# Kernel tuning notes

Measured on AMD Instinct MI355X. Metric: run time of the kernel, lower is better.

Reference implementation:

```python
import jax, jax.numpy as jnp
import numpy as np

HEAD = 3
EMB = 192
MAX_LAYER = 4
NEG_SLOPE_ATT = 0.2
NEG_SLOPE_ACT = 0.1
BN_EPS = 1e-5

def leaky_relu(x, slope):
    return jnp.where(x >= 0, x, slope * x)

def setup_inputs() -> dict:
    key = jax.random.key(0)
    ks = jax.random.split(key, 8)
    N, E, D_IN = 64000, 512000, 128
    k = EMB // HEAD
    subx = jax.random.normal(ks[0], (N, D_IN), dtype=jnp.float32)
    edge_index = jax.random.randint(ks[1], (2, E), 0, N, dtype=jnp.int32)
    mask = jax.random.randint(ks[2], (E, 1), 0, 2, dtype=jnp.int32)
    W = jax.random.normal(ks[3], (EMB, D_IN), dtype=jnp.float32) * (1.0 / np.sqrt(D_IN))
    att = jax.random.normal(ks[4], (1, HEAD, 2 * k), dtype=jnp.float32) * 0.1
    bias = jnp.zeros((EMB,), dtype=jnp.float32)
    gamma = jnp.ones((EMB,), dtype=jnp.float32)
    beta = jnp.zeros((EMB,), dtype=jnp.float32)
    return {"subx": subx, "edge_index": edge_index, "mask": mask, "W": W,
            "att": att, "bias": bias, "gamma": gamma, "beta": beta,
            "batch_size": 32, "subgraph_size": 500}

def reference(subx, edge_index, mask, W, att, bias, gamma, beta, batch_size, subgraph_size):
    N = subx.shape[0]
    k = EMB // HEAD
    # linear projection, split into heads: [N, H, k]
    x = (subx @ W.T).reshape(N, HEAD, k)
    src = edge_index[0]  # softmax grouping index (as in original code)
    dst = edge_index[1]  # aggregation target (PyG source_to_target flow)
    x_i = x[dst]  # [E, H, k]
    x_j = x[src]  # [E, H, k]
    # attention logits per edge per head
    alpha = (jnp.concatenate([x_i, x_j], axis=-1) * att).sum(-1)  # [E, H]
    alpha = leaky_relu(alpha, NEG_SLOPE_ATT)
    # segment softmax grouped by src (faithful to original)
    amax = jax.ops.segment_max(alpha, src, num_segments=N)
    ex = jnp.exp(alpha - amax[src])
    denom = jax.ops.segment_sum(ex, src, num_segments=N)
    alpha = ex / (denom[src] + 1e-16)
    # edge mask (tile over heads)
    m = (mask.reshape(-1, 1, 1) != 0)
    msg = jnp.where(m, x_j, 0.0) * alpha[..., None]  # [E, H, k]
    # scatter-add to target nodes
    aggr = jax.ops.segment_sum(msg, dst, num_segments=N).reshape(N, EMB) + bias
    # LeakyReLU(0.1) then BatchNorm1d (training-mode batch stats)
    h = leaky_relu(aggr, NEG_SLOPE_ACT)
    mean = h.mean(axis=0)
    var = h.var(axis=0)
    h = gamma * (h - mean) / jnp.sqrt(var + BN_EPS) + beta
    # mean over k-hop layers
    h = h.reshape(batch_size, MAX_LAYER, subgraph_size, EMB)
    return h.mean(axis=1)
```

## Files before the change

### kernel.cpp

```cpp
#include <hip/hip_runtime.h>

#define EMBD 192
#define DIN 128
#define SB 1024

__device__ __forceinline__ void f4add(float4& a, const float4& b){
  a.x += b.x; a.y += b.y; a.z += b.z; a.w += b.w;
}

__global__ __launch_bounds__(256) void k_gemm(const float* __restrict__ A,
      const float* __restrict__ W, const float* __restrict__ att,
      float* __restrict__ X, float* __restrict__ ai4, float* __restrict__ aj4,
      unsigned* __restrict__ zbuf, long zcount, int N){
  {
    long i = (long)(blockIdx.y*gridDim.x + blockIdx.x)*blockDim.x + threadIdx.x;
    long st = (long)gridDim.x*gridDim.y*blockDim.x;
    for (; i < zcount; i += st) zbuf[i] = 0u;
  }

  __shared__ float4 Ws[2048];
  int t  = threadIdx.x;
  int nb = blockIdx.y;
  const float4* Wg = (const float4*)W + (size_t)nb*2048;
  #pragma unroll
  for (int i = 0; i < 8; i++){
    int idx = i*256 + t;
    int wr = idx >> 5, wk = idx & 31;
    Ws[wr*32 + (wk ^ ((wr>>3)&7))] = Wg[idx];
  }

  int c = t & 7;
  int r = t >> 3;
  float atti[8], attj[8];
  #pragma unroll
  for (int j = 0; j < 8; j++){
    atti[j] = att[nb*128 + c*8 + j];
    attj[j] = att[nb*128 + 64 + c*8 + j];
  }
  __syncthreads();

  int m0 = blockIdx.x*128 + r*4;
  int mc0 = (m0 + 3 < N) ? m0 : (N > 4 ? N - 4 : 0);
  const float4* Ag = (const float4*)A;

  float acc[4][8];
  #pragma unroll
  for (int rr = 0; rr < 4; rr++)
    #pragma unroll
    for (int j = 0; j < 8; j++) acc[rr][j] = 0.f;

  float4 a_cur[4];
  #pragma unroll
  for (int rr = 0; rr < 4; rr++) a_cur[rr] = Ag[(size_t)(mc0+rr)*32];

  #pragma unroll 4
  for (int k4 = 0; k4 < 32; k4++){
    float4 a_nxt[4];
    if (k4 < 31){
      #pragma unroll
      for (int rr = 0; rr < 4; rr++) a_nxt[rr] = Ag[(size_t)(mc0+rr)*32 + k4 + 1];
    }
    #pragma unroll
    for (int j = 0; j < 8; j++){
      float4 w = Ws[(c*8 + j)*32 + (k4 ^ c)];
      #pragma unroll
      for (int rr = 0; rr < 4; rr++){
        acc[rr][j] += a_cur[rr].x*w.x + a_cur[rr].y*w.y + a_cur[rr].z*w.z + a_cur[rr].w*w.w;
      }
    }
    #pragma unroll
    for (int rr = 0; rr < 4; rr++) a_cur[rr] = a_nxt[rr];
  }

  #pragma unroll
  for (int rr = 0; rr < 4; rr++){
    int m = mc0 + rr;
    float pi = 0.f, pj = 0.f;
    #pragma unroll
    for (int j = 0; j < 8; j++){ pi += acc[rr][j]*atti[j]; pj += acc[rr][j]*attj[j]; }
    pi += __shfl_xor(pi, 1); pi += __shfl_xor(pi, 2); pi += __shfl_xor(pi, 4);
    pj += __shfl_xor(pj, 1); pj += __shfl_xor(pj, 2); pj += __shfl_xor(pj, 4);
    if (m0 + rr < N){
      float4* Xo = (float4*)(X + (size_t)m*EMBD + nb*64 + c*8);
      Xo[0] = make_float4(acc[rr][0], acc[rr][1], acc[rr][2], acc[rr][3]);
      Xo[1] = make_float4(acc[rr][4], acc[rr][5], acc[rr][6], acc[rr][7]);
      if (c == 0){ ai4[(size_t)m*4 + nb] = pi; aj4[(size_t)m*4 + nb] = pj; }
    }
  }
}

__global__ void k_count(const int* __restrict__ ei, const int* __restrict__ msk,
    int* __restrict__ count2, int* __restrict__ slot_src, int* __restrict__ slot_dst,
    int E, int N){
  int e = blockIdx.x*256 + threadIdx.x;
  if (e >= E) return;
  int s = ei[e], d = ei[E + e];
  slot_src[e] = atomicAdd(&count2[s], 1);
  slot_dst[e] = msk[e] ? atomicAdd(&count2[N + d], 1) : -1;
}

__global__ void k_scan1(const int* __restrict__ count, int* __restrict__ offs,
                        int* __restrict__ bsum, int M){
  __shared__ int sm[256];
  int t = threadIdx.x, i = blockIdx.x*256 + t;
  int v = (i < M) ? count[i] : 0;
  sm[t] = v; __syncthreads();
  for (int o = 1; o < 256; o <<= 1){
    int u = (t >= o) ? sm[t-o] : 0;
    __syncthreads();
    sm[t] += u;
    __syncthreads();
  }
  if (i < M) offs[i] = sm[t] - v;
  if (t == 255) bsum[blockIdx.x] = sm[255];
}

__global__ void k_scan2(int* __restrict__ bsum, int NB){
  __shared__ int sm[1024];
  int t = threadIdx.x;
  int v = (t < NB) ? bsum[t] : 0;
  sm[t] = v; __syncthreads();
  for (int o = 1; o < 1024; o <<= 1){
    int u = (t >= o) ? sm[t-o] : 0;
    __syncthreads();
    sm[t] += u;
    __syncthreads();
  }
  if (t < NB) bsum[t] = sm[t] - v;
}

__global__ void k_scan3(int* __restrict__ offs, const int* __restrict__ bsum, int M){
  int i = blockIdx.x*256 + threadIdx.x;
  if (i < M) offs[i] += bsum[blockIdx.x];
}

__global__ void k_fill(const int* __restrict__ ei, const int* __restrict__ slot_src,
    const int* __restrict__ slot_dst, const int* __restrict__ offs2,
    int* __restrict__ elist_src, int* __restrict__ elist_dst, int E, int N){
  int e = blockIdx.x*256 + threadIdx.x;
  if (e >= E) return;
  int s = ei[e], d = ei[E + e];
  elist_src[offs2[s] + slot_src[e]] = d;
  int sd = slot_dst[e];
  if (sd >= 0) elist_dst[offs2[N + d] + sd] = s;
}

__global__ __launch_bounds__(256) void k_denom(const int* __restrict__ count2,
    const int* __restrict__ offs2, const int* __restrict__ elist_src,
    const float4* __restrict__ ai4, const float4* __restrict__ aj4,
    float4* __restrict__ denom4, int N){
  int g = threadIdx.x >> 4, l = threadIdx.x & 15;
  int n = blockIdx.x*16 + g;
  if (n >= N) return;
  int deg = count2[n];
  if (deg == 0) return;
  int base = offs2[n];
  float4 xj = aj4[n];
  float s0 = 0.f, s1 = 0.f, s2 = 0.f;
  for (int j = l; j < deg; j += 16){
    int d = elist_src[base + j];
    float4 xi = ai4[d];
    float a0 = xi.x + xj.x; a0 = a0 >= 0.f ? a0 : 0.2f*a0; s0 += expf(a0);
    float a1 = xi.y + xj.y; a1 = a1 >= 0.f ? a1 : 0.2f*a1; s1 += expf(a1);
    float a2 = xi.z + xj.z; a2 = a2 >= 0.f ? a2 : 0.2f*a2; s2 += expf(a2);
  }
  s0 += __shfl_xor(s0, 1); s0 += __shfl_xor(s0, 2); s0 += __shfl_xor(s0, 4); s0 += __shfl_xor(s0, 8);
  s1 += __shfl_xor(s1, 1); s1 += __shfl_xor(s1, 2); s1 += __shfl_xor(s1, 4); s1 += __shfl_xor(s1, 8);
  s2 += __shfl_xor(s2, 1); s2 += __shfl_xor(s2, 2); s2 += __shfl_xor(s2, 4); s2 += __shfl_xor(s2, 8);
  if (l == 0)
    denom4[n] = make_float4(1.f/(s0 + 1e-16f), 1.f/(s1 + 1e-16f), 1.f/(s2 + 1e-16f), 0.f);
}

__global__ __launch_bounds__(256) void k_aggr(const float* __restrict__ X,
    const int* __restrict__ count2, const int* __restrict__ offs2,
    const int* __restrict__ elist_dst, const float4* __restrict__ ai4,
    const float4* __restrict__ aj4, const float4* __restrict__ denom4,
    const float* __restrict__ bias, float* __restrict__ hact, int N){
  int w = threadIdx.x >> 6, l = threadIdx.x & 63;
  int n = blockIdx.x*4 + w;
  if (n >= N) return;
  int deg = count2[N + n], base = offs2[N + n];
  float4 xi = ai4[n];
  float ac0 = 0.f, ac1 = 0.f, ac2 = 0.f;
  #pragma unroll 4
  for (int j = 0; j < deg; j++){
    int s = elist_dst[base + j];
    float4 xj = aj4[s];
    float4 rn = denom4[s];
    float a0 = xi.x + xj.x; a0 = a0 >= 0.f ? a0 : 0.2f*a0; float c0 = expf(a0)*rn.x;
    float a1 = xi.y + xj.y; a1 = a1 >= 0.f ? a1 : 0.2f*a1; float c1 = expf(a1)*rn.y;
    float a2 = xi.z + xj.z; a2 = a2 >= 0.f ? a2 : 0.2f*a2; float c2 = expf(a2)*rn.z;
    const float* xr = X + (size_t)s*EMBD;
    ac0 += c0 * xr[l];
    ac1 += c1 * xr[64 + l];
    ac2 += c2 * xr[128 + l];
  }
  float* o = hact + (size_t)n*EMBD;
  float v0 = ac0 + bias[l];       v0 = v0 >= 0.f ? v0 : 0.1f*v0; o[l]       = v0;
  float v1 = ac1 + bias[64 + l];  v1 = v1 >= 0.f ? v1 : 0.1f*v1; o[64 + l]  = v1;
  float v2 = ac2 + bias[128 + l]; v2 = v2 >= 0.f ? v2 : 0.1f*v2; o[128 + l] = v2;
}

__global__ __launch_bounds__(192) void k_stat1(const float4* __restrict__ h4,
    float4* __restrict__ part4, int N){
  int t = threadIdx.x;
  int fcol = t % 48, rg = t / 48;
  float4 s = make_float4(0.f,0.f,0.f,0.f);
  float4 q = make_float4(0.f,0.f,0.f,0.f);
  for (int r = blockIdx.x*4 + rg; r < N; r += SB*4){
    float4 v = h4[(size_t)r*48 + fcol];
    s.x += v.x; s.y += v.y; s.z += v.z; s.w += v.w;
    q.x += v.x*v.x; q.y += v.y*v.y; q.z += v.z*v.z; q.w += v.w*v.w;
  }
  __shared__ float4 sms[192], smq[192];
  sms[t] = s; smq[t] = q;
  __syncthreads();
  if (rg < 2){ f4add(sms[t], sms[t+96]); f4add(smq[t], smq[t+96]); }
  __syncthreads();
  if (rg == 0){
    f4add(sms[t], sms[t+48]); f4add(smq[t], smq[t+48]);
    part4[(size_t)blockIdx.x*96 + fcol]      = sms[t];
    part4[(size_t)blockIdx.x*96 + 48 + fcol] = smq[t];
  }
}

__global__ __launch_bounds__(256) void k_stat2(const float4* __restrict__ part4,
    float4* __restrict__ stats4, int N){
  int j = blockIdx.x, t = threadIdx.x;
  float4 s = make_float4(0.f,0.f,0.f,0.f);
  float4 q = make_float4(0.f,0.f,0.f,0.f);
  for (int b = t; b < SB; b += 256){
    f4add(s, part4[(size_t)b*96 + j]);
    f4add(q, part4[(size_t)b*96 + 48 + j]);
  }
  #pragma unroll
  for (int o = 32; o > 0; o >>= 1){
    s.x += __shfl_xor(s.x,o); s.y += __shfl_xor(s.y,o);
    s.z += __shfl_xor(s.z,o); s.w += __shfl_xor(s.w,o);
    q.x += __shfl_xor(q.x,o); q.y += __shfl_xor(q.y,o);
    q.z += __shfl_xor(q.z,o); q.w += __shfl_xor(q.w,o);
  }
  __shared__ float4 ws[4], wq[4];
  int wv = t >> 6;
  if ((t & 63) == 0){ ws[wv] = s; wq[wv] = q; }
  __syncthreads();
  if (t == 0){
    f4add(ws[0], ws[1]); f4add(ws[0], ws[2]); f4add(ws[0], ws[3]);
    f4add(wq[0], wq[1]); f4add(wq[0], wq[2]); f4add(wq[0], wq[3]);
    float inv = 1.f / (float)N;
    float4 mean = make_float4(ws[0].x*inv, ws[0].y*inv, ws[0].z*inv, ws[0].w*inv);
    float4 rstd;
    rstd.x = rsqrtf(wq[0].x*inv - mean.x*mean.x + 1e-5f);
    rstd.y = rsqrtf(wq[0].y*inv - mean.y*mean.y + 1e-5f);
    rstd.z = rsqrtf(wq[0].z*inv - mean.z*mean.z + 1e-5f);
    rstd.w = rsqrtf(wq[0].w*inv - mean.w*mean.w + 1e-5f);
    stats4[j] = mean;
    stats4[48 + j] = rstd;
  }
}

__global__ void k_final(const float* __restrict__ hact, const float* __restrict__ stats,
    const float* __restrict__ gamma, const float* __restrict__ beta,
    const int* __restrict__ sgs, float* __restrict__ out, int total){
  int o = blockIdx.x*256 + threadIdx.x;
  if (o >= total) return;
  int S = *sgs;
  int c  = o % EMBD;
  int rs = o / EMBD;
  int b  = rs / S;
  int s  = rs % S;
  size_t n0 = (size_t)b*4*S + s;
  float v = 0.25f * (hact[(n0      )*EMBD + c] + hact[(n0 +   S)*EMBD + c] +
                     hact[(n0 + 2*S)*EMBD + c] + hact[(n0 + 3*S)*EMBD + c]);
  out[o] = gamma[c] * ((v - stats[c]) * stats[192 + c]) + beta[c];
}

extern "C" void kernel_launch(void* const* d_in, const int* in_sizes, int n_in,
                              void* d_out, int out_size, void* d_ws, size_t ws_size,
                              hipStream_t stream){
  const float* subx  = (const float*)d_in[0];
  const int*   ei    = (const int*)d_in[1];
  const int*   msk   = (const int*)d_in[2];
  const float* W     = (const float*)d_in[3];
  const float* att   = (const float*)d_in[4];
  const float* bias  = (const float*)d_in[5];
  const float* gamma = (const float*)d_in[6];
  const float* beta  = (const float*)d_in[7];
  const int*   sgs   = (const int*)d_in[9];
  float* out = (float*)d_out;

  int N = in_sizes[0] / DIN;
  int E = in_sizes[1] / 2;

  float*  X         = (float*)d_ws;
  float*  hact      = X + (size_t)N*EMBD;
  float*  denom4    = hact + (size_t)N*EMBD;
  float*  ai4       = denom4 + (size_t)N*4;
  float*  aj4       = ai4 + (size_t)N*4;
  int*    count2    = (int*)(aj4 + (size_t)N*4);
  int*    offs2     = count2 + 2*(size_t)N;
  int*    slot_src  = offs2 + 2*(size_t)N;
  int*    slot_dst  = slot_src + E;
  int*    elist_src = slot_dst + E;
  int*    elist_dst = elist_src + E;
  int*    bsum      = elist_dst + E;
  float*  part      = (float*)(bsum + 1024);
  float*  stats     = part + (size_t)SB*96*4;

  int EB  = (E + 255)/256;
  int MB  = (N + 127)/128;
  int M2  = 2*N;
  int NB2 = (M2 + 255)/256;

  k_gemm <<<dim3(MB, 3), 256, 0, stream>>>(subx, W, att, X, ai4, aj4,
                                           (unsigned*)count2, (long)M2, N);
  k_count<<<EB, 256, 0, stream>>>(ei, msk, count2, slot_src, slot_dst, E, N);
  k_scan1<<<NB2, 256, 0, stream>>>(count2, offs2, bsum, M2);
  k_scan2<<<1, 1024, 0, stream>>>(bsum, NB2);
  k_scan3<<<NB2, 256, 0, stream>>>(offs2, bsum, M2);
  k_fill <<<EB, 256, 0, stream>>>(ei, slot_src, slot_dst, offs2, elist_src, elist_dst, E, N);
  k_denom<<<(N + 15)/16, 256, 0, stream>>>(count2, offs2, elist_src,
                                           (const float4*)ai4, (const float4*)aj4,
                                           (float4*)denom4, N);
  k_aggr <<<(N + 3)/4, 256, 0, stream>>>(X, count2, offs2, elist_dst,
                                         (const float4*)ai4, (const float4*)aj4,
                                         (const float4*)denom4, bias, hact, N);
  k_stat1<<<SB, 192, 0, stream>>>((const float4*)hact, (float4*)part, N);
  k_stat2<<<48, 256, 0, stream>>>((const float4*)part, (float4*)stats, N);
  k_final<<<(out_size + 255)/256, 256, 0, stream>>>(hact, stats, gamma, beta, sgs, out, out_size);
}
```

Measured before the change: 279.8 us.

## Move projection GEMM onto bf16 MFMA with split hi/lo precision emulation

Replaces the FP32 FMA projection GEMM with MFMA 16x16x32 bf16 instructions. Each FP32 value is split into bf16 hi and lo parts, and three products (hi*hi, hi*lo, lo*hi) are summed to approximate FP32 accuracy. The grid is flattened with an XCD-aware block remap, and A and W tiles are staged in swizzled LDS per 64-row block. The change is meant to cut GEMM compute time, but it adds conversion work, reloads W for every row block, and gives slightly lower precision than true FP32.

```diff
diff --git a/kernel.cpp b/kernel.cpp
--- a/kernel.cpp
+++ b/kernel.cpp
@@ -4,88 +4,113 @@
 #define DIN 128
 #define SB 1024
 
+typedef __bf16 bfrag __attribute__((ext_vector_type(8)));
+typedef float  f32x4 __attribute__((ext_vector_type(4)));
+
 __device__ __forceinline__ void f4add(float4& a, const float4& b){
   a.x += b.x; a.y += b.y; a.z += b.z; a.w += b.w;
+}
+__device__ __forceinline__ unsigned short f2bf(float f){
+  unsigned u = __float_as_uint(f);
+  unsigned r = u + 0x7fffu + ((u >> 16) & 1u);
+  return (unsigned short)(r >> 16);
+}
+__device__ __forceinline__ float bf2f(unsigned short h){
+  return __uint_as_float(((unsigned)h) << 16);
 }
 
 __global__ __launch_bounds__(256) void k_gemm(const float* __restrict__ A,
       const float* __restrict__ W, const float* __restrict__ att,
       float* __restrict__ X, float* __restrict__ ai4, float* __restrict__ aj4,
-      unsigned* __restrict__ zbuf, long zcount, int N){
+      unsigned* __restrict__ zbuf, long zcount, int N, int G){
   {
-    long i = (long)(blockIdx.y*gridDim.x + blockIdx.x)*blockDim.x + threadIdx.x;
-    long st = (long)gridDim.x*gridDim.y*blockDim.x;
+    long i = (long)blockIdx.x*blockDim.x + threadIdx.x;
+    long st = (long)gridDim.x*blockDim.x;
     for (; i < zcount; i += st) zbuf[i] = 0u;
   }
 
-  __shared__ float4 Ws[2048];
-  int t  = threadIdx.x;
-  int nb = blockIdx.y;
-  const float4* Wg = (const float4*)W + (size_t)nb*2048;
+  int flat = blockIdx.x;
+  int L = (G % 8 == 0) ? ((flat & 7)*(G >> 3) + (flat >> 3)) : flat;
+  int rowblk = L / 3, head = L - rowblk*3;
+
+  __shared__ unsigned short As_hi[8192], As_lo[8192];
+  __shared__ unsigned short Ws_hi[8192], Ws_lo[8192];
+  int t = threadIdx.x;
+
+  const float4* Ag = (const float4*)A;
+  const float4* Wg = (const float4*)W + (size_t)(head*64)*32;
   #pragma unroll
   for (int i = 0; i < 8; i++){
     int idx = i*256 + t;
-    int wr = idx >> 5, wk = idx & 31;
-    Ws[wr*32 + (wk ^ ((wr>>3)&7))] = Wg[idx];
-  }
-
-  int c = t & 7;
-  int r = t >> 3;
-  float atti[8], attj[8];
-  #pragma unroll
-  for (int j = 0; j < 8; j++){
-    atti[j] = att[nb*128 + c*8 + j];
-    attj[j] = att[nb*128 + 64 + c*8 + j];
+    int r = idx >> 5, c4 = idx & 31;
+    int g = (c4 >> 1) ^ (r & 15);
+    int base = (r*16 + g)*8 + (c4 & 1)*4;
+    int row = rowblk*64 + r; if (row >= N) row = N - 1;
+    float4 va = Ag[(size_t)row*32 + c4];
+    float4 vw = Wg[(size_t)idx];
+    unsigned short h; float lo;
+    ushort4 ah, al, wh, wl;
+    h = f2bf(va.x); lo = va.x - bf2f(h); ah.x = h; al.x = f2bf(lo);
+    h = f2bf(va.y); lo = va.y - bf2f(h); ah.y = h; al.y = f2bf(lo);
+    h = f2bf(va.z); lo = va.z - bf2f(h); ah.z = h; al.z = f2bf(lo);
+    h = f2bf(va.w); lo = va.w - bf2f(h); ah.w = h; al.w = f2bf(lo);
+    *(ushort4*)&As_hi[base] = ah; *(ushort4*)&As_lo[base] = al;
+    h = f2bf(vw.x); lo = vw.x - bf2f(h); wh.x = h; wl.x = f2bf(lo);
+    h = f2bf(vw.y); lo = vw.y - bf2f(h); wh.y = h; wl.y = f2bf(lo);
+    h = f2bf(vw.z); lo = vw.z - bf2f(h); wh.z = h; wl.z = f2bf(lo);
+    h = f2bf(vw.w); lo = vw.w - bf2f(h); wh.w = h; wl.w = f2bf(lo);
+    *(ushort4*)&Ws_hi[base] = wh; *(ushort4*)&Ws_lo[base] = wl;
+  }
+
+  int wave = t >> 6, lane = t & 63;
+  int lc = lane & 15, kg = lane >> 4;
+  float atti_l[4], attj_l[4];
+  #pragma unroll
+  for (int ct = 0; ct < 4; ct++){
+    atti_l[ct] = att[head*128 + ct*16 + lc];
+    attj_l[ct] = att[head*128 + 64 + ct*16 + lc];
   }
   __syncthreads();
 
-  int m0 = blockIdx.x*128 + r*4;
-  int mc0 = (m0 + 3 < N) ? m0 : (N > 4 ? N - 4 : 0);
-  const float4* Ag = (const float4*)A;
-
-  float acc[4][8];
-  #pragma unroll
-  for (int rr = 0; rr < 4; rr++)
+  int arow = wave*16 + lc;
+  f32x4 acc[4];
+  #pragma unroll
+  for (int ct = 0; ct < 4; ct++) acc[ct] = (f32x4){0.f, 0.f, 0.f, 0.f};
+
+  #pragma unroll
+  for (int ks = 0; ks < 4; ks++){
+    int g = ks*4 + kg;
+    int aoff = (arow*16 + (g ^ (arow & 15)))*8;
+    bfrag ah = *(const bfrag*)&As_hi[aoff];
+    bfrag al = *(const bfrag*)&As_lo[aoff];
     #pragma unroll
-    for (int j = 0; j < 8; j++) acc[rr][j] = 0.f;
-
-  float4 a_cur[4];
-  #pragma unroll
-  for (int rr = 0; rr < 4; rr++) a_cur[rr] = Ag[(size_t)(mc0+rr)*32];
-
-  #pragma unroll 4
-  for (int k4 = 0; k4 < 32; k4++){
-    float4 a_nxt[4];
-    if (k4 < 31){
-      #pragma unroll
-      for (int rr = 0; rr < 4; rr++) a_nxt[rr] = Ag[(size_t)(mc0+rr)*32 + k4 + 1];
+    for (int ct = 0; ct < 4; ct++){
+      int boff = ((ct*16 + lc)*16 + (g ^ lc))*8;
+      bfrag bh = *(const bfrag*)&Ws_hi[boff];
+      bfrag bl = *(const bfrag*)&Ws_lo[boff];
+      acc[ct] = __builtin_amdgcn_mfma_f32_16x16x32_bf16(ah, bh, acc[ct], 0, 0, 0);
+      acc[ct] = __builtin_amdgcn_mfma_f32_16x16x32_bf16(ah, bl, acc[ct], 0, 0, 0);
+      acc[ct] = __builtin_amdgcn_mfma_f32_16x16x32_bf16(al, bh, acc[ct], 0, 0, 0);
     }
-    #pragma unroll
-    for (int j = 0; j < 8; j++){
-      float4 w = Ws[(c*8 + j)*32 + (k4 ^ c)];
-      #pragma unroll
-      for (int rr = 0; rr < 4; rr++){
-        acc[rr][j] += a_cur[rr].x*w.x + a_cur[rr].y*w.y + a_cur[rr].z*w.z + a_cur[rr].w*w.w;
-      }
-    }
-    #pragma unroll
-    for (int rr = 0; rr < 4; rr++) a_cur[rr] = a_nxt[rr];
-  }
-
-  #pragma unroll
-  for (int rr = 0; rr < 4; rr++){
-    int m = mc0 + rr;
+  }
+
+  int mbase = rowblk*64 + wave*16 + kg*4;
+  #pragma unroll
+  for (int r = 0; r < 4; r++){
+    int m = mbase + r;
+    bool ok = (m < N);
     float pi = 0.f, pj = 0.f;
     #pragma unroll
-    for (int j = 0; j < 8; j++){ pi += acc[rr][j]*atti[j]; pj += acc[rr][j]*attj[j]; }
-    pi += __shfl_xor(pi, 1); pi += __shfl_xor(pi, 2); pi += __shfl_xor(pi, 4);
-    pj += __shfl_xor(pj, 1); pj += __shfl_xor(pj, 2); pj += __shfl_xor(pj, 4);
-    if (m0 + rr < N){
-      float4* Xo = (float4*)(X + (size_t)m*EMBD + nb*64 + c*8);
-      Xo[0] = make_float4(acc[rr][0], acc[rr][1], acc[rr][2], acc[rr][3]);
-      Xo[1] = make_float4(acc[rr][4], acc[rr][5], acc[rr][6], acc[rr][7]);
-      if (c == 0){ ai4[(size_t)m*4 + nb] = pi; aj4[(size_t)m*4 + nb] = pj; }
+    for (int ct = 0; ct < 4; ct++){
+      float v = acc[ct][r];
+      if (ok) X[(size_t)m*EMBD + head*64 + ct*16 + lc] = v;
+      pi += v*atti_l[ct]; pj += v*attj_l[ct];
     }
+    pi += __shfl_xor(pi, 1); pi += __shfl_xor(pi, 2);
+    pi += __shfl_xor(pi, 4); pi += __shfl_xor(pi, 8);
+    pj += __shfl_xor(pj, 1); pj += __shfl_xor(pj, 2);
+    pj += __shfl_xor(pj, 4); pj += __shfl_xor(pj, 8);
+    if (ok && lc == 0){ ai4[(size_t)m*4 + head] = pi; aj4[(size_t)m*4 + head] = pj; }
   }
 }
 
@@ -308,12 +333,13 @@
   float*  stats     = part + (size_t)SB*96*4;
 
   int EB  = (E + 255)/256;
-  int MB  = (N + 127)/128;
+  int MB2 = (N + 63)/64;
+  int G   = MB2*3;
   int M2  = 2*N;
   int NB2 = (M2 + 255)/256;
 
-  k_gemm <<<dim3(MB, 3), 256, 0, stream>>>(subx, W, att, X, ai4, aj4,
-                                           (unsigned*)count2, (long)M2, N);
+  k_gemm <<<G, 256, 0, stream>>>(subx, W, att, X, ai4, aj4,
+                                 (unsigned*)count2, (long)M2, N, G);
   k_count<<<EB, 256, 0, stream>>>(ei, msk, count2, slot_src, slot_dst, E, N);
   k_scan1<<<NB2, 256, 0, stream>>>(count2, offs2, bsum, M2);
   k_scan2<<<1, 1024, 0, stream>>>(bsum, NB2);
```

Measured after the change: 265.3 us. 1.05x faster.
